# Performance work log

Hardware: AMD Instinct MI355X
Metric: run time of the kernel (lower is better)

The kernel has to match this reference:

```python
import jax, jax.numpy as jnp
import numpy as np

NEG_INF = -1e9
ALPHA = 0.2  # LeakyReLU slope


def gat_layer(x, adj, W, a_src, a_dst):
    # x: (N, F), adj: (N, N) bool, W: (F, H, D), a_src/a_dst: (H, D)
    h = jnp.einsum('nf,fhd->nhd', x, W)                 # (N, H, D)
    es = jnp.einsum('nhd,hd->nh', h, a_src)             # score from target node i
    ed = jnp.einsum('nhd,hd->nh', h, a_dst)             # score from neighbor j
    e = jax.nn.leaky_relu(es[:, None, :] + ed[None, :, :], ALPHA)  # (N, N, H)
    e = jnp.where(adj[:, :, None], e, NEG_INF)
    attn = jax.nn.softmax(e, axis=1)                    # softmax over neighbors j
    out = jnp.einsum('ijh,jhd->ihd', attn, h)           # (N, H, D)
    N, H, D = out.shape
    return out.reshape(N, H * D)                        # concat heads


def setup_inputs() -> dict:
    key = jax.random.key(0)
    ks = jax.random.split(key, 8)
    N, F, H1, D1, C = 4096, 512, 8, 8, 16
    node_matrix = jax.random.normal(ks[0], (N, F), dtype=jnp.float32)
    adj = jax.random.bernoulli(ks[1], 0.005, (N, N))
    adj = jnp.logical_or(adj, jnp.eye(N, dtype=bool))   # self-loops
    s1 = 1.0 / np.sqrt(F)
    s2 = 1.0 / np.sqrt(H1 * D1)
    return {
        'node_matrix': node_matrix,
        'adj_matrix': adj,
        'W1': jax.random.normal(ks[2], (F, H1, D1), dtype=jnp.float32) * s1,
        'a1_src': jax.random.normal(ks[3], (H1, D1), dtype=jnp.float32) * s1,
        'a1_dst': jax.random.normal(ks[4], (H1, D1), dtype=jnp.float32) * s1,
        'W2': jax.random.normal(ks[5], (H1 * D1, 1, C), dtype=jnp.float32) * s2,
        'a2_src': jax.random.normal(ks[6], (1, C), dtype=jnp.float32) * s2,
        'a2_dst': jax.random.normal(ks[7], (1, C), dtype=jnp.float32) * s2,
    }


def reference(node_matrix, adj_matrix, W1, a1_src, a1_dst, W2, a2_src, a2_dst):
    # dropout layers are identity in eval mode
    z1 = gat_layer(node_matrix, adj_matrix, W1, a1_src, a1_dst)  # (N, 64)
    a1 = jax.nn.elu(z1)
    z2 = gat_layer(a1, adj_matrix, W2, a2_src, a2_dst)           # (N, num_classes)
    return z2
```

## Files before the change

### kernel.cpp

```cpp
#include <hip/hip_runtime.h>

#define N_NODES 4096
#define F_IN    512
#define NH1     8
#define F1      64
#define C2      16
#define MAXDEG  128

#define GEMM_BLKS 256
#define SCAN_BLKS 1024

__device__ __forceinline__ float wave_sum(float v) {
    for (int o = 32; o >= 1; o >>= 1) v += __shfl_xor(v, o, 64);
    return v;
}

__device__ __forceinline__ int detect_width_wave(const unsigned char* __restrict__ adj,
                                                 int l) {
    bool nz0 = false, nz1 = false, nz2 = false, nz3 = false;
    unsigned int mx = 0u;
    const uint4* p = (const uint4*)adj;
    #pragma unroll
    for (int i = 0; i < 4; ++i) {
        uint4 q = p[l + 64 * i];
        unsigned int wd[4] = {q.x, q.y, q.z, q.w};
        #pragma unroll
        for (int k = 0; k < 4; ++k) {
            unsigned int v = wd[k];
            unsigned int b0 = v & 0xffu, b1 = (v >> 8) & 0xffu;
            unsigned int b2 = (v >> 16) & 0xffu, b3 = (v >> 24) & 0xffu;
            if (b0) { nz0 = true; mx = mx > b0 ? mx : b0; }
            if (b1) { nz1 = true; mx = mx > b1 ? mx : b1; }
            if (b2) { nz2 = true; mx = mx > b2 ? mx : b2; }
            if (b3) { nz3 = true; mx = mx > b3 ? mx : b3; }
        }
    }
    const bool a0 = __any(nz0), a1 = __any(nz1), a2 = __any(nz2), a3 = __any(nz3);
    const bool big = __any(mx > 1u);
    if (!a1 && !a2 && !a3) return 4;
    if (!a0 && !a1)        return 4;
    if (!a0 && !a2)        return 2;
    if (!big)              return 1;
    return 2;
}

__global__ __launch_bounds__(256) void frontend_kernel(
        const unsigned char* __restrict__ adj,
        unsigned short* __restrict__ neigh, int* __restrict__ deg,
        const float* __restrict__ x, const float* __restrict__ W1,
        const float* __restrict__ asrc, const float* __restrict__ adst,
        float* __restrict__ h1, float* __restrict__ es, float* __restrict__ ed) {
    __shared__ __align__(16) float smem[8192 + 4096];
    __shared__ int scnt[4];
    const int t = threadIdx.x;
    const int wv = t >> 6;
    const int l = t & 63;

    if (blockIdx.x < GEMM_BLKS) {
        float* xs = smem;
        float* wt = smem + 8192;
        const int row0 = blockIdx.x * 16;
        {
            const float4* src = (const float4*)(x + (size_t)row0 * F_IN);
            float4* dst = (float4*)xs;
            #pragma unroll
            for (int i = 0; i < 8; ++i) dst[t + i * 256] = src[t + i * 256];
        }
        const float4* w1v = (const float4*)W1;
        float4* wtv = (float4*)wt;
        #pragma unroll
        for (int i = 0; i < 4; ++i) wtv[t + i * 256] = w1v[t + i * 256];

        const int c = l;
        float a0 = 0.f, a1 = 0.f, a2 = 0.f, a3 = 0.f;
        for (int tile = 0; tile < 8; ++tile) {
            __syncthreads();
            float4 pf0, pf1, pf2, pf3;
            if (tile < 7) {
                const float4* s = w1v + (size_t)(tile + 1) * 1024;
                pf0 = s[t]; pf1 = s[t + 256]; pf2 = s[t + 512]; pf3 = s[t + 768];
            }
            const float4* xr0 = (const float4*)&xs[(wv     ) * F_IN + tile * 64];
            const float4* xr1 = (const float4*)&xs[(wv +  4) * F_IN + tile * 64];
            const float4* xr2 = (const float4*)&xs[(wv +  8) * F_IN + tile * 64];
            const float4* xr3 = (const float4*)&xs[(wv + 12) * F_IN + tile * 64];
            #pragma unroll
            for (int kk = 0; kk < 64; kk += 4) {
                float4 x0 = xr0[kk >> 2];
                float4 x1 = xr1[kk >> 2];
                float4 x2 = xr2[kk >> 2];
                float4 x3 = xr3[kk >> 2];
                float w0 = wt[(kk + 0) * 64 + c];
                float w1 = wt[(kk + 1) * 64 + c];
                float w2 = wt[(kk + 2) * 64 + c];
                float w3 = wt[(kk + 3) * 64 + c];
                a0 += x0.x * w0 + x0.y * w1 + x0.z * w2 + x0.w * w3;
                a1 += x1.x * w0 + x1.y * w1 + x1.z * w2 + x1.w * w3;
                a2 += x2.x * w0 + x2.y * w1 + x2.z * w2 + x2.w * w3;
                a3 += x3.x * w0 + x3.y * w1 + x3.z * w2 + x3.w * w3;
            }
            __syncthreads();
            if (tile < 7) {
                wtv[t] = pf0; wtv[t + 256] = pf1;
                wtv[t + 512] = pf2; wtv[t + 768] = pf3;
            }
        }
        float acc[4] = {a0, a1, a2, a3};
        #pragma unroll
        for (int r = 0; r < 4; ++r) {
            const int n = row0 + wv + 4 * r;
            h1[(size_t)n * F1 + c] = acc[r];
            float s = acc[r] * asrc[c];
            float d = acc[r] * adst[c];
            s += __shfl_xor(s, 1); s += __shfl_xor(s, 2); s += __shfl_xor(s, 4);
            d += __shfl_xor(d, 1); d += __shfl_xor(d, 2); d += __shfl_xor(d, 4);
            if ((c & 7) == 0) {
                es[n * NH1 + (c >> 3)] = s;
                ed[n * NH1 + (c >> 3)] = d;
            }
        }
    } else {
        const int w = detect_width_wave(adj, l);
        const int row = (blockIdx.x - GEMM_BLKS) * 4 + wv;
        int* cnt = scnt + wv;
        if (l == 0) *cnt = 0;
        unsigned short* outp = neigh + (size_t)row * MAXDEG;
        if (w == 1) {
            const uint4* p = (const uint4*)(adj + (size_t)row * N_NODES);
            uint4 v[4];
            #pragma unroll
            for (int i = 0; i < 4; ++i) v[i] = p[l + 64 * i];
            #pragma unroll
            for (int i = 0; i < 4; ++i) {
                if ((v[i].x | v[i].y | v[i].z | v[i].w) == 0u) continue;
                unsigned int wd[4] = {v[i].x, v[i].y, v[i].z, v[i].w};
                int base = (l + 64 * i) * 16;
                for (int q = 0; q < 4; ++q) {
                    unsigned int word = wd[q];
                    for (int bb = 0; bb < 4; ++bb) {
                        if ((word >> (8 * bb)) & 0xffu) {
                            int pos = atomicAdd(cnt, 1);
                            if (pos < MAXDEG) outp[pos] = (unsigned short)(base + q * 4 + bb);
                        }
                    }
                }
            }
        } else if (w == 2) {
            const uint4* p = (const uint4*)(adj + (size_t)row * N_NODES * 2);
            uint4 v[8];
            #pragma unroll
            for (int i = 0; i < 8; ++i) v[i] = p[l + 64 * i];
            #pragma unroll
            for (int i = 0; i < 8; ++i) {
                if ((v[i].x | v[i].y | v[i].z | v[i].w) == 0u) continue;
                unsigned int wd[4] = {v[i].x, v[i].y, v[i].z, v[i].w};
                int base = (l + 64 * i) * 8;
                for (int q = 0; q < 4; ++q) {
                    unsigned int word = wd[q];
                    if (word & 0xffffu) {
                        int pos = atomicAdd(cnt, 1);
                        if (pos < MAXDEG) outp[pos] = (unsigned short)(base + q * 2);
                    }
                    if (word >> 16) {
                        int pos = atomicAdd(cnt, 1);
                        if (pos < MAXDEG) outp[pos] = (unsigned short)(base + q * 2 + 1);
                    }
                }
            }
        } else {
            const uint4* p = (const uint4*)(adj + (size_t)row * N_NODES * 4);
            #pragma unroll
            for (int b = 0; b < 2; ++b) {
                uint4 v[8];
                #pragma unroll
                for (int i = 0; i < 8; ++i) v[i] = p[l + 64 * (b * 8 + i)];
                #pragma unroll
                for (int i = 0; i < 8; ++i) {
                    if ((v[i].x | v[i].y | v[i].z | v[i].w) == 0u) continue;
                    unsigned int wd[4] = {v[i].x, v[i].y, v[i].z, v[i].w};
                    int base = (l + 64 * (b * 8 + i)) * 4;
                    for (int q = 0; q < 4; ++q) {
                        if (wd[q]) {
                            int pos = atomicAdd(cnt, 1);
                            if (pos < MAXDEG) outp[pos] = (unsigned short)(base + q);
                        }
                    }
                }
            }
        }
        if (l == 0) deg[row] = min(*cnt, MAXDEG);
    }
}

__global__ __launch_bounds__(256) void attn1_kernel(
        const unsigned short* __restrict__ neigh, const int* __restrict__ deg,
        const float* __restrict__ h1, const float* __restrict__ es,
        const float* __restrict__ ed, const float* __restrict__ W2,
        const float* __restrict__ a2s, const float* __restrict__ a2d,
        float* __restrict__ h2, float* __restrict__ es2, float* __restrict__ ed2) {
    __shared__ float pbufA[4 * 576];
    __shared__ float arowA[4 * 64];
    const int t = threadIdx.x;
    const int wv = t >> 6;
    const int l = t & 63;
    const int i = blockIdx.x * 4 + wv;
    float* pw   = pbufA + wv * 576;
    float* arow = arowA + wv * 64;
    const int hq = l >> 3;

    const int K = deg[i];
    const unsigned short* lst = neigh + (size_t)i * MAXDEG;

    float plsum[NH1];
    #pragma unroll
    for (int h = 0; h < NH1; ++h) plsum[h] = 0.f;
    const float4 e0 = *(const float4*)(es + (size_t)i * NH1);
    const float4 e1 = *(const float4*)(es + (size_t)i * NH1 + 4);
    const float esi[NH1] = {e0.x, e0.y, e0.z, e0.w, e1.x, e1.y, e1.z, e1.w};
    float acc = 0.f;

    for (int t0 = 0; t0 < K; t0 += 64) {
        const int tc = min(64, K - t0);
        const bool valid = l < tc;
        const int j = valid ? (int)lst[t0 + l] : 0;
        const float4 d0v = *(const float4*)(ed + (size_t)j * NH1);
        const float4 d1v = *(const float4*)(ed + (size_t)j * NH1 + 4);
        const float edv[NH1] = {d0v.x, d0v.y, d0v.z, d0v.w,
                                d1v.x, d1v.y, d1v.z, d1v.w};
        #pragma unroll
        for (int h = 0; h < NH1; ++h) {
            float v = esi[h] + edv[h];
            v = (v >= 0.f) ? v : 0.2f * v;
            float p = valid ? __expf(v) : 0.f;
            plsum[h] += p;
            pw[l * 9 + h] = p;
        }
        __builtin_amdgcn_wave_barrier();
        const int tcPad = (tc + 7) & ~7;
        for (int u = 0; u < tcPad; u += 8) {
            #pragma unroll
            for (int vv = 0; vv < 8; ++vv) {
                const int slot = u + vv;
                const int jn = __shfl(j, slot);
                acc += pw[slot * 9 + hq] * h1[(size_t)jn * F1 + l];
            }
        }
        __builtin_amdgcn_wave_barrier();
    }
    float lsum[NH1];
    #pragma unroll
    for (int h = 0; h < NH1; ++h) lsum[h] = wave_sum(plsum[h]);
    float o = acc / lsum[hq];
    float a1v = (o > 0.f) ? o : (__expf(o) - 1.f);

    arow[l] = a1v;
    __builtin_amdgcn_wave_barrier();
    const int cc = l & 15;
    const int kg = l >> 4;
    float hacc = 0.f;
    #pragma unroll
    for (int k = 0; k < 16; ++k)
        hacc += arow[kg * 16 + k] * W2[(kg * 16 + k) * C2 + cc];
    hacc += __shfl_xor(hacc, 16);
    hacc += __shfl_xor(hacc, 32);
    if (l < C2) h2[(size_t)i * C2 + l] = hacc;
    float s2 = hacc * a2s[cc];
    float d2 = hacc * a2d[cc];
    s2 += __shfl_xor(s2, 1); s2 += __shfl_xor(s2, 2);
    s2 += __shfl_xor(s2, 4); s2 += __shfl_xor(s2, 8);
    d2 += __shfl_xor(d2, 1); d2 += __shfl_xor(d2, 2);
    d2 += __shfl_xor(d2, 4); d2 += __shfl_xor(d2, 8);
    if (l == 0) { es2[i] = s2; ed2[i] = d2; }
}

__global__ __launch_bounds__(256) void attn2_kernel(
        const unsigned short* __restrict__ neigh, const int* __restrict__ deg,
        const float* __restrict__ h2, const float* __restrict__ es2,
        const float* __restrict__ ed2, float* __restrict__ out) {
    const int t = threadIdx.x;
    const int wv = t >> 6;
    const int l = t & 63;
    const int i = blockIdx.x * 4 + wv;
    const int c = l & 15;
    const int g = l >> 4;

    const int K = deg[i];
    const unsigned short* lst = neigh + (size_t)i * MAXDEG;

    float plsum = 0.f, acc = 0.f;
    const float esi = es2[i];
    for (int t0 = 0; t0 < K; t0 += 64) {
        const int tc = min(64, K - t0);
        const bool valid = l < tc;
        const int j = valid ? (int)lst[t0 + l] : 0;
        float v = esi + ed2[j];
        v = (v >= 0.f) ? v : 0.2f * v;
        float p = valid ? __expf(v) : 0.f;
        plsum += p;
        const int tcPad = (tc + 3) & ~3;
        for (int u = g; u < tcPad; u += 4) {
            const int jn = __shfl(j, u);
            const float pv = __shfl(p, u);
            acc += pv * h2[(size_t)jn * C2 + c];
        }
    }
    float lsum = wave_sum(plsum);
    acc += __shfl_xor(acc, 16);
    acc += __shfl_xor(acc, 32);
    if (l < C2) out[(size_t)i * C2 + l] = acc / lsum;
}

extern "C" void kernel_launch(void* const* d_in, const int* in_sizes, int n_in,
                              void* d_out, int out_size, void* d_ws, size_t ws_size,
                              hipStream_t stream) {
    const float* x           = (const float*)d_in[0];
    const unsigned char* adj = (const unsigned char*)d_in[1];
    const float* W1          = (const float*)d_in[2];
    const float* a1src       = (const float*)d_in[3];
    const float* a1dst       = (const float*)d_in[4];
    const float* W2          = (const float*)d_in[5];
    const float* a2src       = (const float*)d_in[6];
    const float* a2dst       = (const float*)d_in[7];
    float* out = (float*)d_out;

    char* ws = (char*)d_ws;
    size_t off = 0;
    off += 256;
    unsigned short* neigh = (unsigned short*)(ws + off);
    off += (size_t)N_NODES * MAXDEG * 2;
    int* deg = (int*)(ws + off);                      off += (size_t)N_NODES * 4;
    float* h1 = (float*)(ws + off);                   off += (size_t)N_NODES * F1 * 4;
    float* es1 = (float*)(ws + off);                  off += (size_t)N_NODES * NH1 * 4;
    float* ed1 = (float*)(ws + off);                  off += (size_t)N_NODES * NH1 * 4;
    float* h2 = (float*)(ws + off);                   off += (size_t)N_NODES * C2 * 4;
    float* es2 = (float*)(ws + off);                  off += (size_t)N_NODES * 4;
    float* ed2 = (float*)(ws + off);                  off += (size_t)N_NODES * 4;

    hipLaunchKernelGGL(frontend_kernel, dim3(GEMM_BLKS + SCAN_BLKS), dim3(256), 0, stream,
                       adj, neigh, deg, x, W1, a1src, a1dst, h1, es1, ed1);
    hipLaunchKernelGGL(attn1_kernel, dim3(N_NODES / 4), dim3(256), 0, stream,
                       neigh, deg, h1, es1, ed1, W2, a2src, a2dst, h2, es2, ed2);
    hipLaunchKernelGGL(attn2_kernel, dim3(N_NODES / 4), dim3(256), 0, stream,
                       neigh, deg, h2, es2, ed2, out);
}
```

Measured before the change: 142.2 us.

## Stream W1 tiles via direct global-to-LDS loads and read x rows as scalars

The GEMM part of the frontend kernel stops staging the x rows in shared memory. It reads them directly from global memory through wave-uniform (scalar) addresses, since each wave's rows are the same for all lanes. The W1 tiles are now loaded straight into LDS with global_load_lds instead of a register prefetch followed by a store. This shrinks the LDS footprint and removes the register round trip, but the W1 load is no longer overlapped with compute because it is issued after the barrier, and the x reads become many small scalar loads.

```diff
diff --git a/kernel.cpp b/kernel.cpp
--- a/kernel.cpp
+++ b/kernel.cpp
@@ -13,6 +13,12 @@
 __device__ __forceinline__ float wave_sum(float v) {
     for (int o = 32; o >= 1; o >>= 1) v += __shfl_xor(v, o, 64);
     return v;
+}
+
+typedef __attribute__((address_space(3))) unsigned char lds_uchar;
+typedef __attribute__((address_space(1))) const unsigned char g_uchar;
+__device__ __forceinline__ void gload_lds16(const void* g, void* lds) {
+    __builtin_amdgcn_global_load_lds((g_uchar*)g, (lds_uchar*)lds, 16, 0, 0);
 }
 
 __device__ __forceinline__ int detect_width_wave(const unsigned char* __restrict__ adj,
@@ -50,65 +56,59 @@
         const float* __restrict__ x, const float* __restrict__ W1,
         const float* __restrict__ asrc, const float* __restrict__ adst,
         float* __restrict__ h1, float* __restrict__ es, float* __restrict__ ed) {
-    __shared__ __align__(16) float smem[8192 + 4096];
+    __shared__ __align__(16) float wt[4096];
     __shared__ int scnt[4];
     const int t = threadIdx.x;
     const int wv = t >> 6;
     const int l = t & 63;
 
     if (blockIdx.x < GEMM_BLKS) {
-        float* xs = smem;
-        float* wt = smem + 8192;
         const int row0 = blockIdx.x * 16;
+        const int c = l;
+        const int wvu = __builtin_amdgcn_readfirstlane(wv);
+
         {
-            const float4* src = (const float4*)(x + (size_t)row0 * F_IN);
-            float4* dst = (float4*)xs;
-            #pragma unroll
-            for (int i = 0; i < 8; ++i) dst[t + i * 256] = src[t + i * 256];
-        }
-        const float4* w1v = (const float4*)W1;
-        float4* wtv = (float4*)wt;
-        #pragma unroll
-        for (int i = 0; i < 4; ++i) wtv[t + i * 256] = w1v[t + i * 256];
-
-        const int c = l;
+            const char* src = (const char*)W1;
+            #pragma unroll
+            for (int i2 = 0; i2 < 4; ++i2) {
+                const int seg = wvu * 4 + i2;
+                gload_lds16(src + seg * 1024 + l * 16, (char*)wt + seg * 1024);
+            }
+        }
+
         float a0 = 0.f, a1 = 0.f, a2 = 0.f, a3 = 0.f;
+        const float* xb = x + (size_t)row0 * F_IN;
+        #pragma unroll 1
         for (int tile = 0; tile < 8; ++tile) {
             __syncthreads();
-            float4 pf0, pf1, pf2, pf3;
-            if (tile < 7) {
-                const float4* s = w1v + (size_t)(tile + 1) * 1024;
-                pf0 = s[t]; pf1 = s[t + 256]; pf2 = s[t + 512]; pf3 = s[t + 768];
-            }
-            const float4* xr0 = (const float4*)&xs[(wv     ) * F_IN + tile * 64];
-            const float4* xr1 = (const float4*)&xs[(wv +  4) * F_IN + tile * 64];
-            const float4* xr2 = (const float4*)&xs[(wv +  8) * F_IN + tile * 64];
-            const float4* xr3 = (const float4*)&xs[(wv + 12) * F_IN + tile * 64];
-            #pragma unroll
-            for (int kk = 0; kk < 64; kk += 4) {
-                float4 x0 = xr0[kk >> 2];
-                float4 x1 = xr1[kk >> 2];
-                float4 x2 = xr2[kk >> 2];
-                float4 x3 = xr3[kk >> 2];
-                float w0 = wt[(kk + 0) * 64 + c];
-                float w1 = wt[(kk + 1) * 64 + c];
-                float w2 = wt[(kk + 2) * 64 + c];
-                float w3 = wt[(kk + 3) * 64 + c];
-                a0 += x0.x * w0 + x0.y * w1 + x0.z * w2 + x0.w * w3;
-                a1 += x1.x * w0 + x1.y * w1 + x1.z * w2 + x1.w * w3;
-                a2 += x2.x * w0 + x2.y * w1 + x2.z * w2 + x2.w * w3;
-                a3 += x3.x * w0 + x3.y * w1 + x3.z * w2 + x3.w * w3;
+            const float* xr0 = xb + (size_t)(wvu     ) * F_IN + tile * 64;
+            const float* xr1 = xb + (size_t)(wvu +  4) * F_IN + tile * 64;
+            const float* xr2 = xb + (size_t)(wvu +  8) * F_IN + tile * 64;
+            const float* xr3 = xb + (size_t)(wvu + 12) * F_IN + tile * 64;
+            #pragma unroll
+            for (int kk = 0; kk < 64; kk += 2) {
+                const float w0 = wt[(kk + 0) * 64 + c];
+                const float w1 = wt[(kk + 1) * 64 + c];
+                a0 += xr0[kk] * w0 + xr0[kk + 1] * w1;
+                a1 += xr1[kk] * w0 + xr1[kk + 1] * w1;
+                a2 += xr2[kk] * w0 + xr2[kk + 1] * w1;
+                a3 += xr3[kk] * w0 + xr3[kk + 1] * w1;
             }
             __syncthreads();
             if (tile < 7) {
-                wtv[t] = pf0; wtv[t + 256] = pf1;
-                wtv[t + 512] = pf2; wtv[t + 768] = pf3;
-            }
-        }
+                const char* src = (const char*)W1 + (size_t)(tile + 1) * 16384;
+                #pragma unroll
+                for (int i2 = 0; i2 < 4; ++i2) {
+                    const int seg = wvu * 4 + i2;
+                    gload_lds16(src + seg * 1024 + l * 16, (char*)wt + seg * 1024);
+                }
+            }
+        }
+
         float acc[4] = {a0, a1, a2, a3};
         #pragma unroll
         for (int r = 0; r < 4; ++r) {
-            const int n = row0 + wv + 4 * r;
+            const int n = row0 + wvu + 4 * r;
             h1[(size_t)n * F1 + c] = acc[r];
             float s = acc[r] * asrc[c];
             float d = acc[r] * adst[c];
```

After: 169.6 us. 19.3% more time.

## Split frontend into separate scan and GEMM kernels with ballot-free prefix compaction

Applied to the files above, without the earlier changes.

Splits the fused frontend kernel into two launches: an adjacency scan kernel and a GEMM kernel. The scan now builds a per-lane bitmask with SWAR tricks and uses a wave prefix sum to place neighbor indices in order, replacing per-element shared-memory atomics. The GEMM halves the rows per block (8 instead of 16), doubles the block count, and double-buffers the W1 tile to drop one barrier per tile. This costs an extra kernel launch and removes the overlap of scan and GEMM within one grid, in exchange for cheaper compaction and more GEMM parallelism.

```diff
diff --git a/kernel.cpp b/kernel.cpp
--- a/kernel.cpp
+++ b/kernel.cpp
@@ -7,7 +7,7 @@
 #define C2      16
 #define MAXDEG  128
 
-#define GEMM_BLKS 256
+#define GEMM_BLKS 512
 #define SCAN_BLKS 1024
 
 __device__ __forceinline__ float wave_sum(float v) {
@@ -44,151 +44,160 @@
     return 2;
 }
 
-__global__ __launch_bounds__(256) void frontend_kernel(
+__global__ __launch_bounds__(256) void scan_kernel(
         const unsigned char* __restrict__ adj,
-        unsigned short* __restrict__ neigh, int* __restrict__ deg,
+        unsigned short* __restrict__ neigh, int* __restrict__ deg) {
+    const int t = threadIdx.x;
+    const int wv = t >> 6;
+    const int l = t & 63;
+    const int w = detect_width_wave(adj, l);
+    const int row = blockIdx.x * 4 + wv;
+    unsigned short* outp = neigh + (size_t)row * MAXDEG;
+
+    unsigned long long mask = 0ull;
+    int eshift;
+    if (w == 1) {
+        eshift = 4;
+        const uint4* p = (const uint4*)(adj + (size_t)row * N_NODES);
+        uint4 v[4];
+        #pragma unroll
+        for (int i = 0; i < 4; ++i) v[i] = p[l + 64 * i];
+        #pragma unroll
+        for (int i = 0; i < 4; ++i) {
+            unsigned int wd[4] = {v[i].x, v[i].y, v[i].z, v[i].w};
+            #pragma unroll
+            for (int q = 0; q < 4; ++q) {
+                unsigned int x = wd[q];
+                unsigned int tt = (x | ((x & 0x7f7f7f7fu) + 0x7f7f7f7fu)) & 0x80808080u;
+                unsigned int nib = ((tt >> 7) * 0x01020408u) >> 24;
+                mask |= (unsigned long long)nib << (16 * i + 4 * q);
+            }
+        }
+    } else if (w == 2) {
+        eshift = 3;
+        const uint4* p = (const uint4*)(adj + (size_t)row * N_NODES * 2);
+        uint4 v[8];
+        #pragma unroll
+        for (int i = 0; i < 8; ++i) v[i] = p[l + 64 * i];
+        #pragma unroll
+        for (int i = 0; i < 8; ++i) {
+            unsigned int wd[4] = {v[i].x, v[i].y, v[i].z, v[i].w};
+            #pragma unroll
+            for (int q = 0; q < 4; ++q) {
+                unsigned int x = wd[q];
+                unsigned int b = ((x & 0xffffu) ? 1u : 0u) | ((x >> 16) ? 2u : 0u);
+                mask |= (unsigned long long)b << (8 * i + 2 * q);
+            }
+        }
+    } else {
+        eshift = 2;
+        const uint4* p = (const uint4*)(adj + (size_t)row * N_NODES * 4);
+        #pragma unroll
+        for (int b2 = 0; b2 < 2; ++b2) {
+            uint4 v[8];
+            #pragma unroll
+            for (int i = 0; i < 8; ++i) v[i] = p[l + 64 * (b2 * 8 + i)];
+            #pragma unroll
+            for (int i = 0; i < 8; ++i) {
+                unsigned int wd[4] = {v[i].x, v[i].y, v[i].z, v[i].w};
+                #pragma unroll
+                for (int q = 0; q < 4; ++q)
+                    if (wd[q]) mask |= 1ull << (4 * (b2 * 8 + i) + q);
+            }
+        }
+    }
+
+    const int cnt = __popcll(mask);
+    int pfx = cnt;
+    #pragma unroll
+    for (int o = 1; o < 64; o <<= 1) {
+        int up = __shfl_up(pfx, o, 64);
+        if (l >= o) pfx += up;
+    }
+    int base = pfx - cnt;
+    unsigned long long m = mask;
+    while (m) {
+        const int b = __builtin_ctzll(m);
+        m &= m - 1;
+        const int e = ((b >> eshift) << (eshift + 6)) + (l << eshift)
+                    + (b & ((1 << eshift) - 1));
+        if (base < MAXDEG) outp[base] = (unsigned short)e;
+        ++base;
+    }
+    if (l == 63) deg[row] = min(pfx, MAXDEG);
+}
+
+__global__ __launch_bounds__(256) void gemm_kernel(
         const float* __restrict__ x, const float* __restrict__ W1,
         const float* __restrict__ asrc, const float* __restrict__ adst,
         float* __restrict__ h1, float* __restrict__ es, float* __restrict__ ed) {
-    __shared__ __align__(16) float smem[8192 + 4096];
-    __shared__ int scnt[4];
+    __shared__ __align__(16) float smem[4096 + 2 * 4096];
     const int t = threadIdx.x;
-    const int wv = t >> 6;
-    const int l = t & 63;
-
-    if (blockIdx.x < GEMM_BLKS) {
-        float* xs = smem;
-        float* wt = smem + 8192;
-        const int row0 = blockIdx.x * 16;
-        {
-            const float4* src = (const float4*)(x + (size_t)row0 * F_IN);
-            float4* dst = (float4*)xs;
-            #pragma unroll
-            for (int i = 0; i < 8; ++i) dst[t + i * 256] = src[t + i * 256];
-        }
-        const float4* w1v = (const float4*)W1;
-        float4* wtv = (float4*)wt;
-        #pragma unroll
-        for (int i = 0; i < 4; ++i) wtv[t + i * 256] = w1v[t + i * 256];
-
-        const int c = l;
-        float a0 = 0.f, a1 = 0.f, a2 = 0.f, a3 = 0.f;
-        for (int tile = 0; tile < 8; ++tile) {
-            __syncthreads();
-            float4 pf0, pf1, pf2, pf3;
-            if (tile < 7) {
-                const float4* s = w1v + (size_t)(tile + 1) * 1024;
-                pf0 = s[t]; pf1 = s[t + 256]; pf2 = s[t + 512]; pf3 = s[t + 768];
-            }
-            const float4* xr0 = (const float4*)&xs[(wv     ) * F_IN + tile * 64];
-            const float4* xr1 = (const float4*)&xs[(wv +  4) * F_IN + tile * 64];
-            const float4* xr2 = (const float4*)&xs[(wv +  8) * F_IN + tile * 64];
-            const float4* xr3 = (const float4*)&xs[(wv + 12) * F_IN + tile * 64];
-            #pragma unroll
-            for (int kk = 0; kk < 64; kk += 4) {
-                float4 x0 = xr0[kk >> 2];
-                float4 x1 = xr1[kk >> 2];
-                float4 x2 = xr2[kk >> 2];
-                float4 x3 = xr3[kk >> 2];
-                float w0 = wt[(kk + 0) * 64 + c];
-                float w1 = wt[(kk + 1) * 64 + c];
-                float w2 = wt[(kk + 2) * 64 + c];
-                float w3 = wt[(kk + 3) * 64 + c];
-                a0 += x0.x * w0 + x0.y * w1 + x0.z * w2 + x0.w * w3;
-                a1 += x1.x * w0 + x1.y * w1 + x1.z * w2 + x1.w * w3;
-                a2 += x2.x * w0 + x2.y * w1 + x2.z * w2 + x2.w * w3;
-                a3 += x3.x * w0 + x3.y * w1 + x3.z * w2 + x3.w * w3;
-            }
-            __syncthreads();
-            if (tile < 7) {
-                wtv[t] = pf0; wtv[t + 256] = pf1;
-                wtv[t + 512] = pf2; wtv[t + 768] = pf3;
-            }
-        }
-        float acc[4] = {a0, a1, a2, a3};
-        #pragma unroll
-        for (int r = 0; r < 4; ++r) {
-            const int n = row0 + wv + 4 * r;
-            h1[(size_t)n * F1 + c] = acc[r];
-            float s = acc[r] * asrc[c];
-            float d = acc[r] * adst[c];
-            s += __shfl_xor(s, 1); s += __shfl_xor(s, 2); s += __shfl_xor(s, 4);
-            d += __shfl_xor(d, 1); d += __shfl_xor(d, 2); d += __shfl_xor(d, 4);
-            if ((c & 7) == 0) {
-                es[n * NH1 + (c >> 3)] = s;
-                ed[n * NH1 + (c >> 3)] = d;
-            }
-        }
-    } else {
-        const int w = detect_width_wave(adj, l);
-        const int row = (blockIdx.x - GEMM_BLKS) * 4 + wv;
-        int* cnt = scnt + wv;
-        if (l == 0) *cnt = 0;
-        unsigned short* outp = neigh + (size_t)row * MAXDEG;
-        if (w == 1) {
-            const uint4* p = (const uint4*)(adj + (size_t)row * N_NODES);
-            uint4 v[4];
-            #pragma unroll
-            for (int i = 0; i < 4; ++i) v[i] = p[l + 64 * i];
-            #pragma unroll
-            for (int i = 0; i < 4; ++i) {
-                if ((v[i].x | v[i].y | v[i].z | v[i].w) == 0u) continue;
-                unsigned int wd[4] = {v[i].x, v[i].y, v[i].z, v[i].w};
-                int base = (l + 64 * i) * 16;
-                for (int q = 0; q < 4; ++q) {
-                    unsigned int word = wd[q];
-                    for (int bb = 0; bb < 4; ++bb) {
-                        if ((word >> (8 * bb)) & 0xffu) {
-                            int pos = atomicAdd(cnt, 1);
-                            if (pos < MAXDEG) outp[pos] = (unsigned short)(base + q * 4 + bb);
-                        }
-                    }
-                }
-            }
-        } else if (w == 2) {
-            const uint4* p = (const uint4*)(adj + (size_t)row * N_NODES * 2);
-            uint4 v[8];
-            #pragma unroll
-            for (int i = 0; i < 8; ++i) v[i] = p[l + 64 * i];
-            #pragma unroll
-            for (int i = 0; i < 8; ++i) {
-                if ((v[i].x | v[i].y | v[i].z | v[i].w) == 0u) continue;
-                unsigned int wd[4] = {v[i].x, v[i].y, v[i].z, v[i].w};
-                int base = (l + 64 * i) * 8;
-                for (int q = 0; q < 4; ++q) {
-                    unsigned int word = wd[q];
-                    if (word & 0xffffu) {
-                        int pos = atomicAdd(cnt, 1);
-                        if (pos < MAXDEG) outp[pos] = (unsigned short)(base + q * 2);
-                    }
-                    if (word >> 16) {
-                        int pos = atomicAdd(cnt, 1);
-                        if (pos < MAXDEG) outp[pos] = (unsigned short)(base + q * 2 + 1);
-                    }
-                }
-            }
-        } else {
-            const uint4* p = (const uint4*)(adj + (size_t)row * N_NODES * 4);
-            #pragma unroll
-            for (int b = 0; b < 2; ++b) {
-                uint4 v[8];
-                #pragma unroll
-                for (int i = 0; i < 8; ++i) v[i] = p[l + 64 * (b * 8 + i)];
-                #pragma unroll
-                for (int i = 0; i < 8; ++i) {
-                    if ((v[i].x | v[i].y | v[i].z | v[i].w) == 0u) continue;
-                    unsigned int wd[4] = {v[i].x, v[i].y, v[i].z, v[i].w};
-                    int base = (l + 64 * (b * 8 + i)) * 4;
-                    for (int q = 0; q < 4; ++q) {
-                        if (wd[q]) {
-                            int pos = atomicAdd(cnt, 1);
-                            if (pos < MAXDEG) outp[pos] = (unsigned short)(base + q);
-                        }
-                    }
-                }
-            }
-        }
-        if (l == 0) deg[row] = min(*cnt, MAXDEG);
+
+    float* xs  = smem;
+    float* wt0 = smem + 4096;
+    float* wt1 = smem + 8192;
+    const int row0 = blockIdx.x * 8;
+
+    {
+        const float4* src = (const float4*)(x + (size_t)row0 * F_IN);
+        float4* dst = (float4*)xs;
+        #pragma unroll
+        for (int i = 0; i < 4; ++i) dst[t + i * 256] = src[t + i * 256];
+    }
+    const float4* w1v = (const float4*)W1;
+    {
+        float4* d = (float4*)wt0;
+        #pragma unroll
+        for (int i = 0; i < 4; ++i) d[t + i * 256] = w1v[t + i * 256];
+    }
+
+    const int c = t & 63;
+    const int rq = t >> 6;
+    float a0 = 0.f, a1 = 0.f;
+    float* wcur = wt0;
+    float* wnxt = wt1;
+    for (int tile = 0; tile < 8; ++tile) {
+        __syncthreads();
+        float4 pf0, pf1, pf2, pf3;
+        if (tile < 7) {
+            const float4* s = w1v + (size_t)(tile + 1) * 1024;
+            pf0 = s[t]; pf1 = s[t + 256]; pf2 = s[t + 512]; pf3 = s[t + 768];
+        }
+        const float4* xr0 = (const float4*)&xs[rq * F_IN + tile * 64];
+        const float4* xr1 = (const float4*)&xs[(rq + 4) * F_IN + tile * 64];
+        #pragma unroll
+        for (int kk = 0; kk < 64; kk += 4) {
+            float4 x0 = xr0[kk >> 2];
+            float4 x1 = xr1[kk >> 2];
+            float w0 = wcur[(kk + 0) * 64 + c];
+            float w1 = wcur[(kk + 1) * 64 + c];
+            float w2 = wcur[(kk + 2) * 64 + c];
+            float w3 = wcur[(kk + 3) * 64 + c];
+            a0 += x0.x * w0 + x0.y * w1 + x0.z * w2 + x0.w * w3;
+            a1 += x1.x * w0 + x1.y * w1 + x1.z * w2 + x1.w * w3;
+        }
+        if (tile < 7) {
+            float4* d = (float4*)wnxt;
+            d[t] = pf0; d[t + 256] = pf1; d[t + 512] = pf2; d[t + 768] = pf3;
+        }
+        float* tmp = wcur; wcur = wnxt; wnxt = tmp;
+    }
+
+    const int n0 = row0 + rq;
+    h1[(size_t)n0 * F1 + c] = a0;
+    h1[(size_t)(n0 + 4) * F1 + c] = a1;
+    float s0 = a0 * asrc[c], d0 = a0 * adst[c];
+    float s1 = a1 * asrc[c], d1 = a1 * adst[c];
+    s0 += __shfl_xor(s0, 1); s0 += __shfl_xor(s0, 2); s0 += __shfl_xor(s0, 4);
+    d0 += __shfl_xor(d0, 1); d0 += __shfl_xor(d0, 2); d0 += __shfl_xor(d0, 4);
+    s1 += __shfl_xor(s1, 1); s1 += __shfl_xor(s1, 2); s1 += __shfl_xor(s1, 4);
+    d1 += __shfl_xor(d1, 1); d1 += __shfl_xor(d1, 2); d1 += __shfl_xor(d1, 4);
+    if ((c & 7) == 0) {
+        es[n0 * NH1 + (c >> 3)] = s0;
+        ed[n0 * NH1 + (c >> 3)] = d0;
+        es[(n0 + 4) * NH1 + (c >> 3)] = s1;
+        ed[(n0 + 4) * NH1 + (c >> 3)] = d1;
     }
 }
 
@@ -336,8 +345,10 @@
     float* es2 = (float*)(ws + off);                  off += (size_t)N_NODES * 4;
     float* ed2 = (float*)(ws + off);                  off += (size_t)N_NODES * 4;
 
-    hipLaunchKernelGGL(frontend_kernel, dim3(GEMM_BLKS + SCAN_BLKS), dim3(256), 0, stream,
-                       adj, neigh, deg, x, W1, a1src, a1dst, h1, es1, ed1);
+    hipLaunchKernelGGL(scan_kernel, dim3(SCAN_BLKS), dim3(256), 0, stream,
+                       adj, neigh, deg);
+    hipLaunchKernelGGL(gemm_kernel, dim3(GEMM_BLKS), dim3(256), 0, stream,
+                       x, W1, a1src, a1dst, h1, es1, ed1);
     hipLaunchKernelGGL(attn1_kernel, dim3(N_NODES / 4), dim3(256), 0, stream,
                        neigh, deg, h1, es1, ed1, W2, a2src, a2dst, h2, es2, ed2);
     hipLaunchKernelGGL(attn2_kernel, dim3(N_NODES / 4), dim3(256), 0, stream,
```

Result: faster. 138.0 us (-2.9%).
